# Performance work log

Hardware: AMD Instinct MI355X
Metric: run time of the kernel (lower is better)

The kernel has to match this reference:

```python
import jax, jax.numpy as jnp
import numpy as np

TOTAL_LABELS = 21
TOTAL_POS = 128
TOTAL_NEG = 128
VARIANCES = jnp.asarray([0.1, 0.1, 0.2, 0.2], dtype=jnp.float32)


def _make_boxes(key, shape):
    # valid [y1,x1,y2,x2] boxes with y2>y1, x2>x1 in [0,1]
    k1, k2 = jax.random.split(key)
    lo = jax.random.uniform(k1, shape + (2,), dtype=jnp.float32) * 0.6
    sz = jax.random.uniform(k2, shape + (2,), dtype=jnp.float32) * 0.4 + 1e-3
    return jnp.concatenate([lo, lo + sz], axis=-1)


def setup_inputs() -> dict:
    key = jax.random.key(0)
    kr, kg, kl, kp, kn = jax.random.split(key, 5)
    B, N, M = 64, 3000, 128
    roi_bboxes = _make_boxes(kr, (B, N))
    gt_boxes = _make_boxes(kg, (B, M))
    gt_labels = jax.random.randint(kl, (B, M), 1, TOTAL_LABELS).astype(jnp.int32)
    maxval = max(TOTAL_POS, TOTAL_NEG) * 10  # matches tf.random.uniform(minval=1, maxval=10*count)
    rand_pos = jax.random.randint(kp, (B, N), 1, maxval).astype(jnp.int32)
    rand_neg = jax.random.randint(kn, (B, N), 1, maxval).astype(jnp.int32)
    return {"roi_bboxes": roi_bboxes, "gt_boxes": gt_boxes, "gt_labels": gt_labels,
            "rand_pos": rand_pos, "rand_neg": rand_neg}


def _iou_map(roi, gt):
    # roi: [B,N,4], gt: [B,M,4] -> iou: [B,N,M]
    r = roi[:, :, None, :]
    g = gt[:, None, :, :]
    iy1 = jnp.maximum(r[..., 0], g[..., 0])
    ix1 = jnp.maximum(r[..., 1], g[..., 1])
    iy2 = jnp.minimum(r[..., 2], g[..., 2])
    ix2 = jnp.minimum(r[..., 3], g[..., 3])
    inter = jnp.maximum(iy2 - iy1, 0.0) * jnp.maximum(ix2 - ix1, 0.0)
    area_r = (r[..., 2] - r[..., 0]) * (r[..., 3] - r[..., 1])
    area_g = (g[..., 2] - g[..., 0]) * (g[..., 3] - g[..., 1])
    return inter / (area_r + area_g - inter + 1e-7)


def _random_select(mask, rand_ints, count):
    # faithful port of train_utils.randomly_select_xyz_mask: rank by mask*rand, keep top `count`
    mult = mask.astype(jnp.int32) * rand_ints
    order = jnp.argsort(-mult, axis=-1)
    ranks = jnp.argsort(order, axis=-1)
    return mask & (ranks < count)


def _get_deltas(bboxes, gt):
    bw = bboxes[..., 3] - bboxes[..., 1]
    bh = bboxes[..., 2] - bboxes[..., 0]
    bcx = bboxes[..., 1] + 0.5 * bw
    bcy = bboxes[..., 0] + 0.5 * bh
    gw = gt[..., 3] - gt[..., 1]
    gh = gt[..., 2] - gt[..., 0]
    gcx = gt[..., 1] + 0.5 * gw
    gcy = gt[..., 0] + 0.5 * gh
    bw = jnp.where(bw == 0.0, 1e-3, bw)
    bh = jnp.where(bh == 0.0, 1e-3, bh)
    dx = jnp.where(gw == 0.0, 0.0, (gcx - bcx) / bw)
    dy = jnp.where(gh == 0.0, 0.0, (gcy - bcy) / bh)
    dw = jnp.where(gw == 0.0, 0.0, jnp.log(jnp.where(gw == 0.0, 1.0, gw / bw)))
    dh = jnp.where(gh == 0.0, 0.0, jnp.log(jnp.where(gh == 0.0, 1.0, gh / bh)))
    return jnp.stack([dy, dx, dh, dw], axis=-1)


def reference(roi_bboxes, gt_boxes, gt_labels, rand_pos, rand_neg):
    B, N = roi_bboxes.shape[:2]
    iou = _iou_map(roi_bboxes, gt_boxes)                      # [B,N,M]
    best_gt = jnp.argmax(iou, axis=2)                         # [B,N]
    best_iou = jnp.max(iou, axis=2)                           # [B,N]
    pos_mask = _random_select(best_iou > 0.5, rand_pos, TOTAL_POS)
    neg_mask = _random_select((best_iou < 0.5) & (best_iou > 0.1), rand_neg, TOTAL_NEG)
    gt_boxes_map = jnp.take_along_axis(gt_boxes, best_gt[:, :, None], axis=1)   # [B,N,4]
    expanded_gt_boxes = jnp.where(pos_mask[..., None], gt_boxes_map, 0.0)
    gt_labels_map = jnp.take_along_axis(gt_labels, best_gt, axis=1)             # [B,N]
    pos_gt_labels = jnp.where(pos_mask, gt_labels_map, -1)
    expanded_gt_labels = pos_gt_labels + neg_mask.astype(jnp.int32)
    deltas = _get_deltas(roi_bboxes, expanded_gt_boxes) / VARIANCES             # [B,N,4]
    roi_bbox_labels = jax.nn.one_hot(expanded_gt_labels, TOTAL_LABELS, dtype=deltas.dtype)  # [B,N,L]
    # broadcast-multiply scatter: place deltas into the slot of the assigned label
    roi_bbox_deltas = roi_bbox_labels[..., None] * deltas[:, :, None, :]        # [B,N,L,4]
    roi_bbox_deltas = roi_bbox_deltas.reshape(B, N * TOTAL_LABELS, 4)
    return (jax.lax.stop_gradient(roi_bbox_deltas), jax.lax.stop_gradient(roi_bbox_labels))
```

## Files before the change

### kernel.cpp

```cpp
#include <hip/hip_runtime.h>

#define BB 64
#define NN 3000
#define MM 128
#define NBINS 1280
#define NSEL 128

__global__ __launch_bounds__(256) void k0_zero(float4* __restrict__ o, int n4)
{
  int i = blockIdx.x * 256 + threadIdx.x;
  if (i < n4) o[i] = make_float4(0.f, 0.f, 0.f, 0.f);
}

__global__ __launch_bounds__(256) void k1_iou(
    const float4* __restrict__ roi, const float4* __restrict__ gt,
    const int* __restrict__ gtl, const int* __restrict__ rpos,
    const int* __restrict__ rneg, int* __restrict__ packed,
    float4* __restrict__ deltas)
{
  #pragma clang fp contract(off)
  const int b = blockIdx.y;
  const int n = blockIdx.x * 256 + threadIdx.x;
  const bool valid = (n < NN);
  __shared__ float4 g[MM];
  __shared__ float  ga[MM];
  __shared__ int    gl[MM];

  float4 r = roi[b * NN + (valid ? n : 0)];
  if (threadIdx.x < MM) {
    float4 v = gt[b * MM + threadIdx.x];
    g[threadIdx.x]  = v;
    ga[threadIdx.x] = (v.z - v.x) * (v.w - v.y);
    gl[threadIdx.x] = gtl[b * MM + threadIdx.x];
  }
  __syncthreads();
  if (!valid) return;

  float ar = (r.z - r.x) * (r.w - r.y);
  float best = -1.0f; int bi = 0;
  #pragma unroll 4
  for (int m = 0; m < MM; ++m) {
    float4 gm = g[m];
    float iy1 = fmaxf(r.x, gm.x);
    float ix1 = fmaxf(r.y, gm.y);
    float iy2 = fminf(r.z, gm.z);
    float ix2 = fminf(r.w, gm.w);
    float inter = fmaxf(iy2 - iy1, 0.0f) * fmaxf(ix2 - ix1, 0.0f);
    float iou = inter / (ar + ga[m] - inter + 1e-7f);
    if (iou > best) { best = iou; bi = m; }
  }
  int pm = (best > 0.5f) ? rpos[b * NN + n] : 0;
  int nm = (best < 0.5f && best > 0.1f) ? rneg[b * NN + n] : 0;
  packed[b * NN + n] = pm | (nm << 11) | (gl[bi] << 22);

  float4 gg = g[bi];
  float bw = r.w - r.y, bh = r.z - r.x;
  float bcx = r.y + 0.5f * bw, bcy = r.x + 0.5f * bh;
  float gw = gg.w - gg.y, gh = gg.z - gg.x;
  float gcx = gg.y + 0.5f * gw, gcy = gg.x + 0.5f * gh;
  bw = (bw == 0.0f) ? 0.001f : bw;
  bh = (bh == 0.0f) ? 0.001f : bh;
  float dx = (gw == 0.0f) ? 0.0f : (gcx - bcx) / bw;
  float dy = (gh == 0.0f) ? 0.0f : (gcy - bcy) / bh;
  float dw = (gw == 0.0f) ? 0.0f : logf(gw / bw);
  float dh = (gh == 0.0f) ? 0.0f : logf(gh / bh);
  deltas[b * NN + n] = make_float4(dy / 0.1f, dx / 0.1f, dh / 0.2f, dw / 0.2f);
}

__global__ __launch_bounds__(1024) void k2_select(
    const int* __restrict__ packed, const float4* __restrict__ deltas,
    float4* __restrict__ out1, float* __restrict__ out2)
{
  const int b = blockIdx.x;
  const int tid = threadIdx.x;
  const int lane = tid & 63;
  const int wave = tid >> 6;
  __shared__ int sp[NN];
  __shared__ unsigned hist[NBINS + 1];
  __shared__ unsigned wsum[16];
  __shared__ int sT[4];

  for (int i = tid; i < NBINS + 1; i += 1024) hist[i] = 0;
  if (tid == 0) { sT[0] = 0; sT[1] = 0; sT[2] = 0; sT[3] = 0; }
  __syncthreads();

  for (int i = tid; i < NN; i += 1024) {
    int p = packed[b * NN + i];
    sp[i] = p;
    int pm = p & 0x7FF, nm = (p >> 11) & 0x7FF;
    if (pm) atomicAdd(&hist[pm], 1u);
    if (nm) atomicAdd(&hist[nm], 0x10000u);
  }
  __syncthreads();

  if (wave == 0) {
    unsigned cs[21];
    const int base = 1 + lane * 20;
    cs[20] = 0;
    #pragma unroll
    for (int j = 19; j >= 0; --j) cs[j] = cs[j + 1] + hist[base + j];
    unsigned tot = cs[0];
    unsigned run = tot;
    #pragma unroll
    for (int off = 1; off < 64; off <<= 1) {
      unsigned u = __shfl_down(run, off);
      if (lane + off < 64) run += u;
    }
    unsigned above = run - tot;
    #pragma unroll
    for (int j = 0; j < 20; ++j) {
      int bin = base + j;
      unsigned s  = cs[j] + above;
      unsigned sn = cs[j + 1] + above;
      unsigned ps = s & 0xFFFFu, psn = sn & 0xFFFFu;
      if (ps >= NSEL && psn < NSEL) { sT[0] = bin; sT[1] = NSEL - (int)psn; }
      unsigned ns = s >> 16, nsn = sn >> 16;
      if (ns >= NSEL && nsn < NSEL) { sT[2] = bin; sT[3] = NSEL - (int)nsn; }
    }
  }
  __syncthreads();
  const int Tp = sT[0], Qp = sT[1], Tn = sT[2], Qn = sT[3];

  const int n0 = tid * 3;
  int q[3] = {0, 0, 0};
  if (n0     < NN) q[0] = sp[n0];
  if (n0 + 1 < NN) q[1] = sp[n0 + 1];
  if (n0 + 2 < NN) q[2] = sp[n0 + 2];
  unsigned cc = 0;
  #pragma unroll
  for (int j = 0; j < 3; ++j) {
    int pm = q[j] & 0x7FF, nm = (q[j] >> 11) & 0x7FF;
    if (Tp && pm == Tp) cc += 1u;
    if (Tn && nm == Tn) cc += 0x10000u;
  }
  unsigned inc = cc;
  #pragma unroll
  for (int off = 1; off < 64; off <<= 1) {
    unsigned u = __shfl_up(inc, off);
    if (lane >= off) inc += u;
  }
  if (lane == 63) wsum[wave] = inc;
  __syncthreads();
  unsigned woff = 0;
  for (int w = 0; w < wave; ++w) woff += wsum[w];
  unsigned excl = woff + (inc - cc);
  int ep = (int)(excl & 0xFFFFu), en = (int)(excl >> 16);

  #pragma unroll
  for (int j = 0; j < 3; ++j) {
    int n = n0 + j;
    if (n >= NN) break;
    int p = q[j];
    int pm = p & 0x7FF, nm = (p >> 11) & 0x7FF;
    bool selp;
    if (pm > Tp) selp = true;
    else if (pm && pm == Tp) { selp = (ep < Qp); ep++; }
    else selp = false;
    bool seln;
    if (nm > Tn) seln = true;
    else if (nm && nm == Tn) { seln = (en < Qn); en++; }
    else seln = false;
    if (selp | seln) {
      size_t nl = (size_t)b * NN + n;
      int lab = selp ? ((p >> 22) & 0x1F) : 0;
      out2[nl * 21 + lab] = 1.0f;
      if (lab > 0) out1[nl * 21 + lab] = deltas[nl];
    }
  }
}

extern "C" void kernel_launch(void* const* d_in, const int* in_sizes, int n_in,
                              void* d_out, int out_size, void* d_ws, size_t ws_size,
                              hipStream_t stream) {
  const float4* roi = (const float4*)d_in[0];
  const float4* gt  = (const float4*)d_in[1];
  const int* gtl  = (const int*)d_in[2];
  const int* rpos = (const int*)d_in[3];
  const int* rneg = (const int*)d_in[4];

  char* ws = (char*)d_ws;
  int*    packed = (int*)ws;
  float4* deltas = (float4*)(ws + (1 << 20));

  float4* out1 = (float4*)d_out;
  float*  out2 = (float*)d_out + (size_t)BB * NN * 21 * 4;

  const int n4 = (BB * NN * 21 * 5) / 4;
  k0_zero<<<(n4 + 255) / 256, 256, 0, stream>>>((float4*)d_out, n4);
  dim3 g1((NN + 255) / 256, BB);
  k1_iou<<<g1, 256, 0, stream>>>(roi, gt, gtl, rpos, rneg, packed, deltas);
  k2_select<<<BB, 1024, 0, stream>>>(packed, deltas, out1, out2);
}
```

Measured before the change: 47.45 us.

## Merge output zeroing into IoU kernel via block specialization

Folds the separate zero-fill kernel into the IoU kernel, reserving the first 1024 blocks as grid-stride zeroers and the rest as IoU/delta compute blocks. The aim is to remove one kernel launch and let the memory-bound zero fill overlap with the compute-bound IoU loop on different CUs. The risk is that zero blocks, dispatched first, may delay the compute blocks, and fewer zero threads may not saturate write bandwidth.

New measurement: 47.03 us, median of 2. About the same (-0.9%).

```diff
diff --git a/kernel.cpp b/kernel.cpp
--- a/kernel.cpp
+++ b/kernel.cpp
@@ -5,33 +5,40 @@
 #define MM 128
 #define NBINS 1280
 #define NSEL 128
+#define ZB 1024
+#define CB (BB * 12)
 
-__global__ __launch_bounds__(256) void k0_zero(float4* __restrict__ o, int n4)
-{
-  int i = blockIdx.x * 256 + threadIdx.x;
-  if (i < n4) o[i] = make_float4(0.f, 0.f, 0.f, 0.f);
-}
-
-__global__ __launch_bounds__(256) void k1_iou(
+__global__ __launch_bounds__(256) void kA(
     const float4* __restrict__ roi, const float4* __restrict__ gt,
     const int* __restrict__ gtl, const int* __restrict__ rpos,
     const int* __restrict__ rneg, int* __restrict__ packed,
-    float4* __restrict__ deltas)
+    float4* __restrict__ deltas, float4* __restrict__ outz)
 {
   #pragma clang fp contract(off)
-  const int b = blockIdx.y;
-  const int n = blockIdx.x * 256 + threadIdx.x;
+  const int tid = threadIdx.x;
+
+  if (blockIdx.x < ZB) {
+    const float4 z = make_float4(0.f, 0.f, 0.f, 0.f);
+    const int total4 = BB * NN * 21 * 5 / 4;
+    for (int i = blockIdx.x * 256 + tid; i < total4; i += ZB * 256)
+      outz[i] = z;
+    return;
+  }
+
+  const int cb = blockIdx.x - ZB;
+  const int b = cb / 12;
+  const int n = (cb % 12) * 256 + tid;
   const bool valid = (n < NN);
   __shared__ float4 g[MM];
   __shared__ float  ga[MM];
   __shared__ int    gl[MM];
 
   float4 r = roi[b * NN + (valid ? n : 0)];
-  if (threadIdx.x < MM) {
-    float4 v = gt[b * MM + threadIdx.x];
-    g[threadIdx.x]  = v;
-    ga[threadIdx.x] = (v.z - v.x) * (v.w - v.y);
-    gl[threadIdx.x] = gtl[b * MM + threadIdx.x];
+  if (tid < MM) {
+    float4 v = gt[b * MM + tid];
+    g[tid]  = v;
+    ga[tid] = (v.z - v.x) * (v.w - v.y);
+    gl[tid] = gtl[b * MM + tid];
   }
   __syncthreads();
   if (!valid) return;
@@ -67,7 +74,7 @@
   deltas[b * NN + n] = make_float4(dy / 0.1f, dx / 0.1f, dh / 0.2f, dw / 0.2f);
 }
 
-__global__ __launch_bounds__(1024) void k2_select(
+__global__ __launch_bounds__(1024) void kB(
     const int* __restrict__ packed, const float4* __restrict__ deltas,
     float4* __restrict__ out1, float* __restrict__ out2)
 {
@@ -185,9 +192,7 @@
   float4* out1 = (float4*)d_out;
   float*  out2 = (float*)d_out + (size_t)BB * NN * 21 * 4;
 
-  const int n4 = (BB * NN * 21 * 5) / 4;
-  k0_zero<<<(n4 + 255) / 256, 256, 0, stream>>>((float4*)d_out, n4);
-  dim3 g1((NN + 255) / 256, BB);
-  k1_iou<<<g1, 256, 0, stream>>>(roi, gt, gtl, rpos, rneg, packed, deltas);
-  k2_select<<<BB, 1024, 0, stream>>>(packed, deltas, out1, out2);
+  kA<<<ZB + CB, 256, 0, stream>>>(roi, gt, gtl, rpos, rneg, packed, deltas,
+                                  (float4*)d_out);
+  kB<<<BB, 1024, 0, stream>>>(packed, deltas, out1, out2);
 }
```
